# Kernel tuning notes

Hardware: AMD Instinct MI355X
Metric: run time of the kernel (lower is better)

The kernel has to match this reference:

```python
import jax, jax.numpy as jnp
import numpy as np

VOCAB = 32
UTT_LEN = 16
NUM_MEANING_TYPES = 5
MEANINGS_PER_TYPE = 10
SUPPORT_SIZE = 100000  # = MEANINGS_PER_TYPE ** NUM_MEANING_TYPES
BATCH = 2048


def setup_inputs() -> dict:
    key = jax.random.key(0)
    k1, k2, k3 = jax.random.split(key, 3)
    # query utterances: [utt_len, batch] token ids
    utts = jax.random.randint(k1, (UTT_LEN, BATCH), 0, VOCAB, dtype=jnp.int64)
    # support set is stored as one-hot encoded utterances [S, utt_len*vocab]
    support_tokens = jax.random.randint(k2, (SUPPORT_SIZE, UTT_LEN), 0, VOCAB)
    support = jax.nn.one_hot(support_tokens, VOCAB, dtype=jnp.float32)
    support = support.reshape(SUPPORT_SIZE, UTT_LEN * VOCAB)
    # meanings table [S, num_meaning_types]
    meanings_t = jax.random.randint(k3, (SUPPORT_SIZE, NUM_MEANING_TYPES), 0,
                                    MEANINGS_PER_TYPE, dtype=jnp.int64)
    return {"utts": utts, "support": support, "meanings_t": meanings_t}


def reference(utts, support, meanings_t):
    # utts: [M, N] ints; support: [S, M*V] floats; meanings_t: [S, T] ints
    M, N = utts.shape
    # one-hot encode queries: [N, M, V] -> [N, M*V]
    batch_fluffy = jax.nn.one_hot(utts.T, VOCAB, dtype=jnp.float32).reshape(N, M * VOCAB)
    batch_sq = jnp.sum(batch_fluffy * batch_fluffy, axis=1)        # [N]
    support_sq = jnp.sum(support * support, axis=1)                # [S]
    cross = batch_fluffy @ support.T                                # [N, S]
    squared_dist = batch_sq[:, None] + support_sq[None, :] - 2.0 * cross
    # top-1 smallest distance (K=1)
    top1 = jnp.argmin(squared_dist, axis=1)                         # [N]
    meanings = meanings_t[top1]                                     # [N, T]
    return jax.nn.one_hot(meanings, MEANINGS_PER_TYPE, dtype=jnp.float32)
```

## Files before the change

kernel.cpp:

```cpp
#include <hip/hip_runtime.h>
#include <stdint.h>

#define S_ROWS 100000
#define NQ     2048
#define M_POS  16
#define VOCABS 32
#define WPB    8
#define GROUPS 8
#define CHUNKS 125
#define RC     800
#define KITER  25
#define KPAD   264

__global__ __launch_bounds__(256) void knn_decode(const float* __restrict__ support,
                                                  uint8_t* __restrict__ tok,
                                                  uint32_t* __restrict__ best) {
    if (blockIdx.x < 8) best[blockIdx.x * 256 + threadIdx.x] = 0u;
    int wave = (blockIdx.x * 256 + threadIdx.x) >> 6;
    int lane = threadIdx.x & 63;
    if (wave >= S_ROWS) return;
    const float4* rowp = (const float4*)(support + (size_t)wave * 512) + lane * 2;
    float4 f0 = rowp[0];
    float4 f1 = rowp[1];
    float base = (float)((lane & 3) * 64);
    float v = f0.x * (base + 0.f)  + f0.y * (base + 8.f)  + f0.z * (base + 16.f) + f0.w * (base + 24.f)
            + f1.x * (base + 32.f) + f1.y * (base + 40.f) + f1.z * (base + 48.f) + f1.w * (base + 56.f);
    v += __shfl_xor(v, 1);
    v += __shfl_xor(v, 2);
    if ((lane & 3) == 0) {
        int p = lane >> 2;
        tok[(size_t)wave * 16 + p] = (uint8_t)(v + 0.5f);
    }
}

__device__ __forceinline__ void FA(uint32_t a, uint32_t b, uint32_t c,
                                   uint32_t& s, uint32_t& co) {
    uint32_t x = a ^ b;
    s  = x ^ c;
    co = (a & b) | (x & c);
}
__device__ __forceinline__ void HA(uint32_t a, uint32_t b, uint32_t& s, uint32_t& co) {
    s = a ^ b; co = a & b;
}

__global__ __launch_bounds__(256, 4) void knn_score(const int* __restrict__ utts,
                                                    const uint8_t* __restrict__ tok,
                                                    uint32_t* __restrict__ best) {
    __shared__ uint32_t smem[32 * KPAD];
    uint32_t* table = smem;
    uint32_t* keys  = smem;

    const int bid = blockIdx.x;
    const int g   = bid & 7;
    const int c   = bid >> 3;
    const int t   = threadIdx.x;

    #pragma unroll
    for (int i = 0; i < 16; ++i) table[t + 256 * i] = 0u;
    __syncthreads();

    {
        int q = g * 256 + t;
        int wb = t >> 5, j = t & 31;
        #pragma unroll
        for (int m = 0; m < M_POS; ++m) {
            int v = utts[m * NQ + q];
            atomicOr(&table[(m * VOCABS + v) * WPB + wb], 1u << j);
        }
    }
    __syncthreads();

    const int w   = t & 7;
    const int sub = t >> 3;
    const int r0  = c * RC;
    const uint32_t* tw = table + w;

    uint32_t cp0=0,cp1=0,cp2=0,cp3=0,cp4=0;
    uint32_t k0p=0,k1p=0,k2p=0,k3p=0,k4p=0;

    const uint4* tbase = (const uint4*)(tok + (size_t)(r0 + sub) * 16);

    #pragma unroll 5
    for (int k = 0; k < KITER; ++k) {
        uint4 ta = tbase[32 * k];
        uint32_t b[16];
        b[0]  = tw[ (ta.x        & 0xFFu) +  0*256];
        b[1]  = tw[((ta.x >> 8)  & 0xFFu) +  1*256];
        b[2]  = tw[((ta.x >> 16) & 0xFFu) +  2*256];
        b[3]  = tw[((ta.x >> 24)        ) +  3*256];
        b[4]  = tw[ (ta.y        & 0xFFu) +  4*256];
        b[5]  = tw[((ta.y >> 8)  & 0xFFu) +  5*256];
        b[6]  = tw[((ta.y >> 16) & 0xFFu) +  6*256];
        b[7]  = tw[((ta.y >> 24)        ) +  7*256];
        b[8]  = tw[ (ta.z        & 0xFFu) +  8*256];
        b[9]  = tw[((ta.z >> 8)  & 0xFFu) +  9*256];
        b[10] = tw[((ta.z >> 16) & 0xFFu) + 10*256];
        b[11] = tw[((ta.z >> 24)        ) + 11*256];
        b[12] = tw[ (ta.w        & 0xFFu) + 12*256];
        b[13] = tw[((ta.w >> 8)  & 0xFFu) + 13*256];
        b[14] = tw[((ta.w >> 16) & 0xFFu) + 14*256];
        b[15] = tw[((ta.w >> 24)        ) + 15*256];

        uint32_t s10,s11,s12,s13,s14, c10,c11,c12,c13,c14;
        FA(b[0],b[1],b[2],   s10,c10);
        FA(b[3],b[4],b[5],   s11,c11);
        FA(b[6],b[7],b[8],   s12,c12);
        FA(b[9],b[10],b[11], s13,c13);
        FA(b[12],b[13],b[14],s14,c14);
        uint32_t s2a,c2a,s2b,c2b;
        FA(s10,s11,s12, s2a,c2a);
        FA(s13,s14,b[15], s2b,c2b);
        uint32_t n0,h0;  HA(s2a,s2b, n0,h0);
        uint32_t u,cu,vv,cv,x2,cx,n1,cy;
        FA(c10,c11,c12, u,cu);
        FA(c13,c14,c2a, vv,cv);
        FA(u,vv,c2b,    x2,cx);
        HA(x2,h0,       n1,cy);
        uint32_t y4,cz,n2,cw,n3,n4;
        FA(cu,cv,cx, y4,cz);
        HA(y4,cy,    n2,cw);
        HA(cz,cw,    n3,n4);

        uint32_t eq = ~(n4 ^ cp4);
        uint32_t gt = n4 & ~cp4;
        gt |= eq & (n3 & ~cp3);  eq &= ~(n3 ^ cp3);
        gt |= eq & (n2 & ~cp2);  eq &= ~(n2 ^ cp2);
        gt |= eq & (n1 & ~cp1);  eq &= ~(n1 ^ cp1);
        gt |= eq & (n0 & ~cp0);

        uint32_t ng = ~gt;
        cp0 = (gt & n0) | (ng & cp0);
        cp1 = (gt & n1) | (ng & cp1);
        cp2 = (gt & n2) | (ng & cp2);
        cp3 = (gt & n3) | (ng & cp3);
        cp4 = (gt & n4) | (ng & cp4);
        uint32_t kb0 = 0u - (uint32_t)( k        & 1);
        uint32_t kb1 = 0u - (uint32_t)((k >> 1)  & 1);
        uint32_t kb2 = 0u - (uint32_t)((k >> 2)  & 1);
        uint32_t kb3 = 0u - (uint32_t)((k >> 3)  & 1);
        uint32_t kb4 = 0u - (uint32_t)((k >> 4)  & 1);
        k0p = (k0p & ng) | (gt & kb0);
        k1p = (k1p & ng) | (gt & kb1);
        k2p = (k2p & ng) | (gt & kb2);
        k3p = (k3p & ng) | (gt & kb3);
        k4p = (k4p & ng) | (gt & kb4);
    }

    __syncthreads();

    {
        uint32_t C = 0x1FFFFu - (uint32_t)(r0 + sub);
        #pragma unroll
        for (int j = 0; j < 32; ++j) {
            uint32_t cnt = ((cp0>>j)&1u) | (((cp1>>j)&1u)<<1) | (((cp2>>j)&1u)<<2)
                         | (((cp3>>j)&1u)<<3) | (((cp4>>j)&1u)<<4);
            uint32_t kk  = ((k0p>>j)&1u) | (((k1p>>j)&1u)<<1) | (((k2p>>j)&1u)<<2)
                         | (((k3p>>j)&1u)<<3) | (((k4p>>j)&1u)<<4);
            uint32_t key = (cnt << 17) + C - (kk << 5);
            keys[j * KPAD + t] = key;
        }
    }
    __syncthreads();

    {
        int w2 = t & 7, j2 = t >> 3;
        const uint32_t* kp = keys + j2 * KPAD + w2;
        uint32_t bestv = 0;
        #pragma unroll
        for (int i = 0; i < 32; ++i) {
            uint32_t v = kp[8 * i];
            bestv = bestv > v ? bestv : v;
        }
        atomicMax(&best[g * 256 + w2 * 32 + j2], bestv);
    }
}

__global__ __launch_bounds__(256) void knn_out(const uint32_t* __restrict__ best,
                                               const int* __restrict__ meanings,
                                               float* __restrict__ out) {
    int q = blockIdx.x * 256 + threadIdx.x;
    if (q >= NQ) return;
    uint32_t b = best[q];
    int idx = 0x1FFFF - (int)(b & 0x1FFFFu);
    float* o = out + (size_t)q * 50;
    #pragma unroll
    for (int tt = 0; tt < 5; ++tt) {
        int mv = meanings[(size_t)idx * 5 + tt];
        #pragma unroll
        for (int mm = 0; mm < 10; ++mm) o[tt * 10 + mm] = (mm == mv) ? 1.0f : 0.0f;
    }
}

extern "C" void kernel_launch(void* const* d_in, const int* in_sizes, int n_in,
                              void* d_out, int out_size, void* d_ws, size_t ws_size,
                              hipStream_t stream) {
    const int*   utts     = (const int*)d_in[0];
    const float* support  = (const float*)d_in[1];
    const int*   meanings = (const int*)d_in[2];
    float* out = (float*)d_out;

    uint8_t*  tok  = (uint8_t*)d_ws;
    uint32_t* best = (uint32_t*)((char*)d_ws + (size_t)S_ROWS * 16);

    knn_decode<<<(S_ROWS + 3) / 4, 256, 0, stream>>>(support, tok, best);
    knn_score<<<GROUPS * CHUNKS, 256, 0, stream>>>(utts, tok, best);
    knn_out<<<NQ / 256, 256, 0, stream>>>(best, meanings, out);
}
```

Baseline: 313.0 us.

## Fuse support decoding into scoring kernel with double-buffered token pipeline

Merges the decode and score kernels into one 1024-thread kernel. Each block decodes its own support rows from global memory into a double-buffered LDS token buffer while the previous row group is scored, and each block now covers all 2048 queries in a 128KB bitmask table. The separate token array round-trip through global memory is removed and best is zeroed with a memset. In exchange each iteration needs a block-wide barrier, occupancy is limited by the large LDS footprint, and only 250 blocks are launched.

```diff
diff --git a/kernel.cpp b/kernel.cpp
--- a/kernel.cpp
+++ b/kernel.cpp
@@ -5,101 +5,95 @@
 #define NQ     2048
 #define M_POS  16
 #define VOCABS 32
-#define WPB    8
-#define GROUPS 8
-#define CHUNKS 125
-#define RC     800
+#define NWORD  64
+#define NBLK   250
+#define RPB    400
+#define RITER  16
 #define KITER  25
-#define KPAD   264
-
-__global__ __launch_bounds__(256) void knn_decode(const float* __restrict__ support,
-                                                  uint8_t* __restrict__ tok,
-                                                  uint32_t* __restrict__ best) {
-    if (blockIdx.x < 8) best[blockIdx.x * 256 + threadIdx.x] = 0u;
-    int wave = (blockIdx.x * 256 + threadIdx.x) >> 6;
-    int lane = threadIdx.x & 63;
-    if (wave >= S_ROWS) return;
-    const float4* rowp = (const float4*)(support + (size_t)wave * 512) + lane * 2;
-    float4 f0 = rowp[0];
-    float4 f1 = rowp[1];
+#define TPB    1024
+
+__device__ __forceinline__ void FA(uint32_t a, uint32_t b, uint32_t c,
+                                   uint32_t& s, uint32_t& co) {
+    uint32_t x = a ^ b;
+    s  = x ^ c;
+    co = (a & b) | (x & c);
+}
+__device__ __forceinline__ void HA(uint32_t a, uint32_t b, uint32_t& s, uint32_t& co) {
+    s = a ^ b; co = a & b;
+}
+
+__device__ __forceinline__ void decode_row(float4 f0, float4 f1, int lane,
+                                           uint8_t* __restrict__ dst) {
     float base = (float)((lane & 3) * 64);
     float v = f0.x * (base + 0.f)  + f0.y * (base + 8.f)  + f0.z * (base + 16.f) + f0.w * (base + 24.f)
             + f1.x * (base + 32.f) + f1.y * (base + 40.f) + f1.z * (base + 48.f) + f1.w * (base + 56.f);
     v += __shfl_xor(v, 1);
     v += __shfl_xor(v, 2);
-    if ((lane & 3) == 0) {
-        int p = lane >> 2;
-        tok[(size_t)wave * 16 + p] = (uint8_t)(v + 0.5f);
-    }
-}
-
-__device__ __forceinline__ void FA(uint32_t a, uint32_t b, uint32_t c,
-                                   uint32_t& s, uint32_t& co) {
-    uint32_t x = a ^ b;
-    s  = x ^ c;
-    co = (a & b) | (x & c);
-}
-__device__ __forceinline__ void HA(uint32_t a, uint32_t b, uint32_t& s, uint32_t& co) {
-    s = a ^ b; co = a & b;
-}
-
-__global__ __launch_bounds__(256, 4) void knn_score(const int* __restrict__ utts,
-                                                    const uint8_t* __restrict__ tok,
+    if ((lane & 3) == 0) dst[lane >> 2] = (uint8_t)(v + 0.5f);
+}
+
+__global__ __launch_bounds__(TPB, 4) void knn_fused(const int* __restrict__ utts,
+                                                    const float* __restrict__ support,
                                                     uint32_t* __restrict__ best) {
-    __shared__ uint32_t smem[32 * KPAD];
-    uint32_t* table = smem;
-    uint32_t* keys  = smem;
-
-    const int bid = blockIdx.x;
-    const int g   = bid & 7;
-    const int c   = bid >> 3;
-    const int t   = threadIdx.x;
+    __shared__ uint32_t smem[M_POS * VOCABS * NWORD];
+    __shared__ __align__(16) uint8_t tokbuf[2][RITER * 16];
+
+    const int t    = threadIdx.x;
+    const int c    = blockIdx.x;
+    const int r0   = c * RPB;
+    const int w    = t & 63;
+    const int sub  = t >> 6;
+    const int lane = t & 63;
 
     #pragma unroll
-    for (int i = 0; i < 16; ++i) table[t + 256 * i] = 0u;
+    for (int i = 0; i < 32; ++i) smem[t + 1024 * i] = 0u;
     __syncthreads();
 
-    {
-        int q = g * 256 + t;
-        int wb = t >> 5, j = t & 31;
+    #pragma unroll
+    for (int qq = 0; qq < 2; ++qq) {
+        int q  = t + qq * 1024;
+        int wb = q >> 5, j = q & 31;
         #pragma unroll
         for (int m = 0; m < M_POS; ++m) {
             int v = utts[m * NQ + q];
-            atomicOr(&table[(m * VOCABS + v) * WPB + wb], 1u << j);
-        }
-    }
+            atomicOr(&smem[(m * VOCABS + v) * NWORD + wb], 1u << j);
+        }
+    }
+
+    const float4* gp = (const float4*)(support + (size_t)(r0 + sub) * 512) + lane * 2;
+    float4 f0 = gp[0];
+    float4 f1 = gp[1];
+    gp += 2048;
+    decode_row(f0, f1, lane, &tokbuf[0][sub * 16]);
+    f0 = gp[0];
+    f1 = gp[1];
+    gp += 2048;
     __syncthreads();
-
-    const int w   = t & 7;
-    const int sub = t >> 3;
-    const int r0  = c * RC;
-    const uint32_t* tw = table + w;
 
     uint32_t cp0=0,cp1=0,cp2=0,cp3=0,cp4=0;
     uint32_t k0p=0,k1p=0,k2p=0,k3p=0,k4p=0;
-
-    const uint4* tbase = (const uint4*)(tok + (size_t)(r0 + sub) * 16);
+    const uint32_t* tw = smem + w;
 
     #pragma unroll 5
-    for (int k = 0; k < KITER; ++k) {
-        uint4 ta = tbase[32 * k];
+    for (int i = 0; i < KITER; ++i) {
+        uint4 ta = *(const uint4*)&tokbuf[i & 1][sub * 16];
         uint32_t b[16];
-        b[0]  = tw[ (ta.x        & 0xFFu) +  0*256];
-        b[1]  = tw[((ta.x >> 8)  & 0xFFu) +  1*256];
-        b[2]  = tw[((ta.x >> 16) & 0xFFu) +  2*256];
-        b[3]  = tw[((ta.x >> 24)        ) +  3*256];
-        b[4]  = tw[ (ta.y        & 0xFFu) +  4*256];
-        b[5]  = tw[((ta.y >> 8)  & 0xFFu) +  5*256];
-        b[6]  = tw[((ta.y >> 16) & 0xFFu) +  6*256];
-        b[7]  = tw[((ta.y >> 24)        ) +  7*256];
-        b[8]  = tw[ (ta.z        & 0xFFu) +  8*256];
-        b[9]  = tw[((ta.z >> 8)  & 0xFFu) +  9*256];
-        b[10] = tw[((ta.z >> 16) & 0xFFu) + 10*256];
-        b[11] = tw[((ta.z >> 24)        ) + 11*256];
-        b[12] = tw[ (ta.w        & 0xFFu) + 12*256];
-        b[13] = tw[((ta.w >> 8)  & 0xFFu) + 13*256];
-        b[14] = tw[((ta.w >> 16) & 0xFFu) + 14*256];
-        b[15] = tw[((ta.w >> 24)        ) + 15*256];
+        b[0]  = tw[ (ta.x        & 0xFFu) * 8 +  0*2048];
+        b[1]  = tw[((ta.x >> 8)  & 0xFFu) * 8 +  1*2048];
+        b[2]  = tw[((ta.x >> 16) & 0xFFu) * 8 +  2*2048];
+        b[3]  = tw[((ta.x >> 24)        ) * 8 +  3*2048];
+        b[4]  = tw[ (ta.y        & 0xFFu) * 8 +  4*2048];
+        b[5]  = tw[((ta.y >> 8)  & 0xFFu) * 8 +  5*2048];
+        b[6]  = tw[((ta.y >> 16) & 0xFFu) * 8 +  6*2048];
+        b[7]  = tw[((ta.y >> 24)        ) * 8 +  7*2048];
+        b[8]  = tw[ (ta.z        & 0xFFu) * 8 +  8*2048];
+        b[9]  = tw[((ta.z >> 8)  & 0xFFu) * 8 +  9*2048];
+        b[10] = tw[((ta.z >> 16) & 0xFFu) * 8 + 10*2048];
+        b[11] = tw[((ta.z >> 24)        ) * 8 + 11*2048];
+        b[12] = tw[ (ta.w        & 0xFFu) * 8 + 12*2048];
+        b[13] = tw[((ta.w >> 8)  & 0xFFu) * 8 + 13*2048];
+        b[14] = tw[((ta.w >> 16) & 0xFFu) * 8 + 14*2048];
+        b[15] = tw[((ta.w >> 24)        ) * 8 + 15*2048];
 
         uint32_t s10,s11,s12,s13,s14, c10,c11,c12,c13,c14;
         FA(b[0],b[1],b[2],   s10,c10);
@@ -134,44 +128,56 @@
         cp2 = (gt & n2) | (ng & cp2);
         cp3 = (gt & n3) | (ng & cp3);
         cp4 = (gt & n4) | (ng & cp4);
-        uint32_t kb0 = 0u - (uint32_t)( k        & 1);
-        uint32_t kb1 = 0u - (uint32_t)((k >> 1)  & 1);
-        uint32_t kb2 = 0u - (uint32_t)((k >> 2)  & 1);
-        uint32_t kb3 = 0u - (uint32_t)((k >> 3)  & 1);
-        uint32_t kb4 = 0u - (uint32_t)((k >> 4)  & 1);
+        uint32_t kb0 = 0u - (uint32_t)( i       & 1);
+        uint32_t kb1 = 0u - (uint32_t)((i >> 1) & 1);
+        uint32_t kb2 = 0u - (uint32_t)((i >> 2) & 1);
+        uint32_t kb3 = 0u - (uint32_t)((i >> 3) & 1);
+        uint32_t kb4 = 0u - (uint32_t)((i >> 4) & 1);
         k0p = (k0p & ng) | (gt & kb0);
         k1p = (k1p & ng) | (gt & kb1);
         k2p = (k2p & ng) | (gt & kb2);
         k3p = (k3p & ng) | (gt & kb3);
         k4p = (k4p & ng) | (gt & kb4);
-    }
-
-    __syncthreads();
+
+        if (i + 1 < KITER) {
+            decode_row(f0, f1, lane, &tokbuf[(i + 1) & 1][sub * 16]);
+            if (i + 2 < KITER) {
+                f0 = gp[0];
+                f1 = gp[1];
+                gp += 2048;
+            }
+        }
+        __syncthreads();
+    }
 
     {
-        uint32_t C = 0x1FFFFu - (uint32_t)(r0 + sub);
+        uint32_t C  = 0x1FFFFu - (uint32_t)(r0 + sub);
+        int       wp = (w + sub) & 63;
         #pragma unroll
         for (int j = 0; j < 32; ++j) {
             uint32_t cnt = ((cp0>>j)&1u) | (((cp1>>j)&1u)<<1) | (((cp2>>j)&1u)<<2)
                          | (((cp3>>j)&1u)<<3) | (((cp4>>j)&1u)<<4);
             uint32_t kk  = ((k0p>>j)&1u) | (((k1p>>j)&1u)<<1) | (((k2p>>j)&1u)<<2)
                          | (((k3p>>j)&1u)<<3) | (((k4p>>j)&1u)<<4);
-            uint32_t key = (cnt << 17) + C - (kk << 5);
-            keys[j * KPAD + t] = key;
+            uint32_t key = (cnt << 17) + C - (kk << 4);
+            smem[j * 1024 + sub * 64 + wp] = key;
         }
     }
     __syncthreads();
 
     {
-        int w2 = t & 7, j2 = t >> 3;
-        const uint32_t* kp = keys + j2 * KPAD + w2;
-        uint32_t bestv = 0;
-        #pragma unroll
-        for (int i = 0; i < 32; ++i) {
-            uint32_t v = kp[8 * i];
-            bestv = bestv > v ? bestv : v;
-        }
-        atomicMax(&best[g * 256 + w2 * 32 + j2], bestv);
+        int w2 = t & 63;
+        #pragma unroll
+        for (int jj = 0; jj < 2; ++jj) {
+            int j2 = (t >> 6) * 2 + jj;
+            uint32_t bestv = 0;
+            #pragma unroll
+            for (int s = 0; s < 16; ++s) {
+                uint32_t v = smem[j2 * 1024 + s * 64 + ((w2 + s) & 63)];
+                bestv = bestv > v ? bestv : v;
+            }
+            atomicMax(&best[w2 * 32 + j2], bestv);
+        }
     }
 }
 
@@ -199,10 +205,9 @@
     const int*   meanings = (const int*)d_in[2];
     float* out = (float*)d_out;
 
-    uint8_t*  tok  = (uint8_t*)d_ws;
-    uint32_t* best = (uint32_t*)((char*)d_ws + (size_t)S_ROWS * 16);
-
-    knn_decode<<<(S_ROWS + 3) / 4, 256, 0, stream>>>(support, tok, best);
-    knn_score<<<GROUPS * CHUNKS, 256, 0, stream>>>(utts, tok, best);
+    uint32_t* best = (uint32_t*)d_ws;
+
+    hipMemsetAsync(best, 0, NQ * sizeof(uint32_t), stream);
+    knn_fused<<<NBLK, TPB, 0, stream>>>(utts, support, best);
     knn_out<<<NQ / 256, 256, 0, stream>>>(best, meanings, out);
 }
```

New measurement: 382.4 us. 1.22x slower.

## Shrink score chunks, halve LDS, prefetch next token row for occupancy

Applied to the files above, without the earlier changes.

Splits the support set into five times more chunks (160 rows each, 5 iterations per thread), so the grid has many more blocks and each thread tracks only 3 bits of the winning-iteration index. Shared memory is halved by doing the key reduction in two 16-bit passes. The next token row is prefetched one iteration ahead, and a waves-per-eu hint is added to raise occupancy. In exchange the number of atomicMax operations on the best array and the table build per block grow fivefold.

```diff
diff --git a/kernel.cpp b/kernel.cpp
--- a/kernel.cpp
+++ b/kernel.cpp
@@ -7,9 +7,9 @@
 #define VOCABS 32
 #define WPB    8
 #define GROUPS 8
-#define CHUNKS 125
-#define RC     800
-#define KITER  25
+#define CHUNKS 625
+#define RC     160
+#define KITER  5
 #define KPAD   264
 
 __global__ __launch_bounds__(256) void knn_decode(const float* __restrict__ support,
@@ -43,10 +43,76 @@
     s = a ^ b; co = a & b;
 }
 
-__global__ __launch_bounds__(256, 4) void knn_score(const int* __restrict__ utts,
-                                                    const uint8_t* __restrict__ tok,
-                                                    uint32_t* __restrict__ best) {
-    __shared__ uint32_t smem[32 * KPAD];
+__device__ __forceinline__ void gather16(const uint32_t* __restrict__ tw, uint4 ta,
+                                         uint32_t b[16]) {
+    b[0]  = tw[ (ta.x        & 0xFFu) +  0*256];
+    b[1]  = tw[((ta.x >> 8)  & 0xFFu) +  1*256];
+    b[2]  = tw[((ta.x >> 16) & 0xFFu) +  2*256];
+    b[3]  = tw[((ta.x >> 24)        ) +  3*256];
+    b[4]  = tw[ (ta.y        & 0xFFu) +  4*256];
+    b[5]  = tw[((ta.y >> 8)  & 0xFFu) +  5*256];
+    b[6]  = tw[((ta.y >> 16) & 0xFFu) +  6*256];
+    b[7]  = tw[((ta.y >> 24)        ) +  7*256];
+    b[8]  = tw[ (ta.z        & 0xFFu) +  8*256];
+    b[9]  = tw[((ta.z >> 8)  & 0xFFu) +  9*256];
+    b[10] = tw[((ta.z >> 16) & 0xFFu) + 10*256];
+    b[11] = tw[((ta.z >> 24)        ) + 11*256];
+    b[12] = tw[ (ta.w        & 0xFFu) + 12*256];
+    b[13] = tw[((ta.w >> 8)  & 0xFFu) + 13*256];
+    b[14] = tw[((ta.w >> 16) & 0xFFu) + 14*256];
+    b[15] = tw[((ta.w >> 24)        ) + 15*256];
+}
+
+__device__ __forceinline__ void score_row(const uint32_t b[16], int k,
+        uint32_t& cp0, uint32_t& cp1, uint32_t& cp2, uint32_t& cp3, uint32_t& cp4,
+        uint32_t& k0p, uint32_t& k1p, uint32_t& k2p) {
+    uint32_t s10,s11,s12,s13,s14, c10,c11,c12,c13,c14;
+    FA(b[0],b[1],b[2],   s10,c10);
+    FA(b[3],b[4],b[5],   s11,c11);
+    FA(b[6],b[7],b[8],   s12,c12);
+    FA(b[9],b[10],b[11], s13,c13);
+    FA(b[12],b[13],b[14],s14,c14);
+    uint32_t s2a,c2a,s2b,c2b;
+    FA(s10,s11,s12, s2a,c2a);
+    FA(s13,s14,b[15], s2b,c2b);
+    uint32_t n0,h0;  HA(s2a,s2b, n0,h0);
+    uint32_t u,cu,vv,cv,x2,cx,n1,cy;
+    FA(c10,c11,c12, u,cu);
+    FA(c13,c14,c2a, vv,cv);
+    FA(u,vv,c2b,    x2,cx);
+    HA(x2,h0,       n1,cy);
+    uint32_t y4,cz,n2,cw,n3,n4;
+    FA(cu,cv,cx, y4,cz);
+    HA(y4,cy,    n2,cw);
+    HA(cz,cw,    n3,n4);
+
+    uint32_t eq = ~(n4 ^ cp4);
+    uint32_t gt = n4 & ~cp4;
+    gt |= eq & (n3 & ~cp3);  eq &= ~(n3 ^ cp3);
+    gt |= eq & (n2 & ~cp2);  eq &= ~(n2 ^ cp2);
+    gt |= eq & (n1 & ~cp1);  eq &= ~(n1 ^ cp1);
+    gt |= eq & (n0 & ~cp0);
+
+    uint32_t ng = ~gt;
+    cp0 = (gt & n0) | (ng & cp0);
+    cp1 = (gt & n1) | (ng & cp1);
+    cp2 = (gt & n2) | (ng & cp2);
+    cp3 = (gt & n3) | (ng & cp3);
+    cp4 = (gt & n4) | (ng & cp4);
+    uint32_t kb0 = 0u - (uint32_t)( k       & 1);
+    uint32_t kb1 = 0u - (uint32_t)((k >> 1) & 1);
+    uint32_t kb2 = 0u - (uint32_t)((k >> 2) & 1);
+    k0p = (k0p & ng) | (gt & kb0);
+    k1p = (k1p & ng) | (gt & kb1);
+    k2p = (k2p & ng) | (gt & kb2);
+}
+
+__global__ __launch_bounds__(256)
+__attribute__((amdgpu_waves_per_eu(4, 8)))
+void knn_score(const int* __restrict__ utts,
+               const uint8_t* __restrict__ tok,
+               uint32_t* __restrict__ best) {
+    __shared__ uint32_t smem[16 * KPAD];
     uint32_t* table = smem;
     uint32_t* keys  = smem;
 
@@ -76,102 +142,48 @@
     const uint32_t* tw = table + w;
 
     uint32_t cp0=0,cp1=0,cp2=0,cp3=0,cp4=0;
-    uint32_t k0p=0,k1p=0,k2p=0,k3p=0,k4p=0;
+    uint32_t k0p=0,k1p=0,k2p=0;
 
     const uint4* tbase = (const uint4*)(tok + (size_t)(r0 + sub) * 16);
 
-    #pragma unroll 5
+    uint4 tA = tbase[0];
+    #pragma unroll 1
     for (int k = 0; k < KITER; ++k) {
-        uint4 ta = tbase[32 * k];
+        int kn = (k + 1 < KITER) ? k + 1 : k;
+        uint4 tAn = tbase[32 * kn];
         uint32_t b[16];
-        b[0]  = tw[ (ta.x        & 0xFFu) +  0*256];
-        b[1]  = tw[((ta.x >> 8)  & 0xFFu) +  1*256];
-        b[2]  = tw[((ta.x >> 16) & 0xFFu) +  2*256];
-        b[3]  = tw[((ta.x >> 24)        ) +  3*256];
-        b[4]  = tw[ (ta.y        & 0xFFu) +  4*256];
-        b[5]  = tw[((ta.y >> 8)  & 0xFFu) +  5*256];
-        b[6]  = tw[((ta.y >> 16) & 0xFFu) +  6*256];
-        b[7]  = tw[((ta.y >> 24)        ) +  7*256];
-        b[8]  = tw[ (ta.z        & 0xFFu) +  8*256];
-        b[9]  = tw[((ta.z >> 8)  & 0xFFu) +  9*256];
-        b[10] = tw[((ta.z >> 16) & 0xFFu) + 10*256];
-        b[11] = tw[((ta.z >> 24)        ) + 11*256];
-        b[12] = tw[ (ta.w        & 0xFFu) + 12*256];
-        b[13] = tw[((ta.w >> 8)  & 0xFFu) + 13*256];
-        b[14] = tw[((ta.w >> 16) & 0xFFu) + 14*256];
-        b[15] = tw[((ta.w >> 24)        ) + 15*256];
-
-        uint32_t s10,s11,s12,s13,s14, c10,c11,c12,c13,c14;
-        FA(b[0],b[1],b[2],   s10,c10);
-        FA(b[3],b[4],b[5],   s11,c11);
-        FA(b[6],b[7],b[8],   s12,c12);
-        FA(b[9],b[10],b[11], s13,c13);
-        FA(b[12],b[13],b[14],s14,c14);
-        uint32_t s2a,c2a,s2b,c2b;
-        FA(s10,s11,s12, s2a,c2a);
-        FA(s13,s14,b[15], s2b,c2b);
-        uint32_t n0,h0;  HA(s2a,s2b, n0,h0);
-        uint32_t u,cu,vv,cv,x2,cx,n1,cy;
-        FA(c10,c11,c12, u,cu);
-        FA(c13,c14,c2a, vv,cv);
-        FA(u,vv,c2b,    x2,cx);
-        HA(x2,h0,       n1,cy);
-        uint32_t y4,cz,n2,cw,n3,n4;
-        FA(cu,cv,cx, y4,cz);
-        HA(y4,cy,    n2,cw);
-        HA(cz,cw,    n3,n4);
-
-        uint32_t eq = ~(n4 ^ cp4);
-        uint32_t gt = n4 & ~cp4;
-        gt |= eq & (n3 & ~cp3);  eq &= ~(n3 ^ cp3);
-        gt |= eq & (n2 & ~cp2);  eq &= ~(n2 ^ cp2);
-        gt |= eq & (n1 & ~cp1);  eq &= ~(n1 ^ cp1);
-        gt |= eq & (n0 & ~cp0);
-
-        uint32_t ng = ~gt;
-        cp0 = (gt & n0) | (ng & cp0);
-        cp1 = (gt & n1) | (ng & cp1);
-        cp2 = (gt & n2) | (ng & cp2);
-        cp3 = (gt & n3) | (ng & cp3);
-        cp4 = (gt & n4) | (ng & cp4);
-        uint32_t kb0 = 0u - (uint32_t)( k        & 1);
-        uint32_t kb1 = 0u - (uint32_t)((k >> 1)  & 1);
-        uint32_t kb2 = 0u - (uint32_t)((k >> 2)  & 1);
-        uint32_t kb3 = 0u - (uint32_t)((k >> 3)  & 1);
-        uint32_t kb4 = 0u - (uint32_t)((k >> 4)  & 1);
-        k0p = (k0p & ng) | (gt & kb0);
-        k1p = (k1p & ng) | (gt & kb1);
-        k2p = (k2p & ng) | (gt & kb2);
-        k3p = (k3p & ng) | (gt & kb3);
-        k4p = (k4p & ng) | (gt & kb4);
+        gather16(tw, tA, b);
+        score_row(b, k, cp0,cp1,cp2,cp3,cp4, k0p,k1p,k2p);
+        tA = tAn;
     }
 
     __syncthreads();
 
-    {
-        uint32_t C = 0x1FFFFu - (uint32_t)(r0 + sub);
+    uint32_t C = 0x1FFFFu - (uint32_t)(r0 + sub);
+    #pragma unroll
+    for (int P = 0; P < 2; ++P) {
         #pragma unroll
-        for (int j = 0; j < 32; ++j) {
+        for (int jj = 0; jj < 16; ++jj) {
+            int j = P * 16 + jj;
             uint32_t cnt = ((cp0>>j)&1u) | (((cp1>>j)&1u)<<1) | (((cp2>>j)&1u)<<2)
                          | (((cp3>>j)&1u)<<3) | (((cp4>>j)&1u)<<4);
-            uint32_t kk  = ((k0p>>j)&1u) | (((k1p>>j)&1u)<<1) | (((k2p>>j)&1u)<<2)
-                         | (((k3p>>j)&1u)<<3) | (((k4p>>j)&1u)<<4);
+            uint32_t kk  = ((k0p>>j)&1u) | (((k1p>>j)&1u)<<1) | (((k2p>>j)&1u)<<2);
             uint32_t key = (cnt << 17) + C - (kk << 5);
-            keys[j * KPAD + t] = key;
+            keys[jj * KPAD + t] = key;
         }
-    }
-    __syncthreads();
-
-    {
-        int w2 = t & 7, j2 = t >> 3;
-        const uint32_t* kp = keys + j2 * KPAD + w2;
-        uint32_t bestv = 0;
-        #pragma unroll
-        for (int i = 0; i < 32; ++i) {
-            uint32_t v = kp[8 * i];
-            bestv = bestv > v ? bestv : v;
+        __syncthreads();
+        {
+            int w2 = t & 7, jr = (t >> 3) & 15, sh = t >> 7;
+            const uint32_t* kp = keys + jr * KPAD + sh * 128 + w2;
+            uint32_t bv = 0;
+            #pragma unroll
+            for (int i = 0; i < 16; ++i) {
+                uint32_t v = kp[8 * i];
+                bv = bv > v ? bv : v;
+            }
+            atomicMax(&best[g * 256 + w2 * 32 + P * 16 + jr], bv);
         }
-        atomicMax(&best[g * 256 + w2 * 32 + j2], bestv);
+        __syncthreads();
     }
 }
 
```

After: 342.3 us. +9.3%, slower.
